# Kernel tuning notes

Measured on AMD Instinct MI355X. Metric: run time of the kernel, lower is better.

Reference implementation:

```python
import jax, jax.numpy as jnp
import numpy as np

N_NODES = 100000
N_EDGES = 1600000
D = 32
K = 3  # Chebyshev kernels
NEG_SLOPE = 0.2


def setup_inputs() -> dict:
    key = jax.random.key(0)
    ks = jax.random.split(key, 10)
    s = 1.0 / np.sqrt(D)
    return {
        "u": jax.random.normal(ks[0], (N_NODES, D), jnp.float32),
        "lambda_max": jnp.full((1,), 2.0, jnp.float32),
        "edge_src": jax.random.randint(ks[1], (N_EDGES,), 0, N_NODES, jnp.int32),
        "edge_dst": jax.random.randint(ks[2], (N_EDGES,), 0, N_NODES, jnp.int32),
        "cheb_W": jax.random.normal(ks[3], (K * D, D), jnp.float32) * s,
        "cheb_b": jnp.zeros((D,), jnp.float32),
        "src_W": jax.random.normal(ks[4], (D, D), jnp.float32) * s,
        "src_b": jnp.zeros((D,), jnp.float32),
        "dst_W": jax.random.normal(ks[5], (D, D), jnp.float32) * s,
        "dst_b": jnp.zeros((D,), jnp.float32),
        "attn": jax.random.normal(ks[6], (1, D), jnp.float32) * s,  # (heads=1, D)
    }


def reference(u, lambda_max, edge_src, edge_dst, cheb_W, cheb_b,
              src_W, src_b, dst_W, dst_b, attn):
    N = u.shape[0]
    # in-degrees (DGL: clamp(min=1) ** -0.5)
    deg = jnp.zeros((N,), u.dtype).at[edge_dst].add(1.0)
    Dinv = jnp.clip(deg, 1.0, None) ** -0.5  # (N,)

    def unnL(x):  # D^{-1/2} A D^{-1/2} x  via copy_u->sum message passing
        m = (x * Dinv[:, None])[edge_src]                       # (E, D)
        agg = jax.ops.segment_sum(m, edge_dst, num_segments=N)  # (N, D)
        return agg * Dinv[:, None]

    # --- ChebConv ---
    re_norm = 2.0 / lambda_max  # (1,) broadcast over all nodes
    X0 = u
    Xt = [X0]
    X1 = X0
    if K > 1:
        h = unnL(X0)
        X1 = -re_norm * h + X0 * (re_norm - 1.0)
        Xt.append(X1)
    for _ in range(2, K):
        h = unnL(X1)
        Xi = -2.0 * re_norm * h + X1 * (2.0 * (re_norm - 1.0)) - X0
        Xt.append(Xi)
        X0, X1 = X1, Xi
    Xcat = jnp.concatenate(Xt, axis=1)                 # (N, K*D)
    hc = jax.nn.relu(Xcat @ cheb_W + cheb_b)           # (N, D), DGL default activation=relu

    # --- GATv2Conv (heads=1) ---
    H = attn.shape[0]
    fsrc = (hc @ src_W + src_b).reshape(N, H, -1)      # (N, H, D)
    fdst = (hc @ dst_W + dst_b).reshape(N, H, -1)
    e = jax.nn.leaky_relu(fsrc[edge_src] + fdst[edge_dst], NEG_SLOPE)  # (E, H, D)
    logits = jnp.einsum('ehd,hd->eh', e, attn)         # (E, H)
    mx = jax.ops.segment_max(logits, edge_dst, num_segments=N)
    mx = jnp.where(jnp.isfinite(mx), mx, 0.0)
    ex = jnp.exp(logits - mx[edge_dst])
    den = jax.ops.segment_sum(ex, edge_dst, num_segments=N)
    a = ex / jnp.where(den > 0, den, 1.0)[edge_dst]    # edge softmax over dst groups
    msg = fsrc[edge_src] * a[:, :, None]               # (E, H, D)
    out = jax.ops.segment_sum(msg, edge_dst, num_segments=N)  # (N, H, D)
    return out.squeeze(1)
```

## Files before the change

kernel.cpp:

```cpp
#include <hip/hip_runtime.h>
#include <hip/hip_bf16.h>


typedef unsigned short u16;

#define DD 32
#define NEG_SLOPE 0.2f
#define BLK 256
#define TILE 4096
#define CB_SHIFT 8
#define CB_NODES 256
#define SRC_BITS 17

#define OFF_CHEBW 0
#define OFF_CHEBB 3072
#define OFF_SRCW  3104
#define OFF_SRCB  4128
#define OFF_DSTW  4160
#define OFF_DSTB  5184
#define OFF_ATTN  5216
#define OFF_LMAX  5248
#define W_TOTAL   5249

#define F_U     0
#define F_CHEBW 1
#define F_CHEBB 2
#define F_SRCW  3
#define F_SRCB  4
#define F_DSTW  5
#define F_DSTB  6
#define F_ATTN  7
#define F_LMAX  8
#define N_FLAGS 9

__device__ __forceinline__ float bh2f(u16 h) {
    return __uint_as_float(((unsigned)h) << 16);
}
__device__ __forceinline__ float rdin(const void* p, long long i, int f32f) {
    return f32f ? ((const float*)p)[i] : bh2f(((const u16*)p)[i]);
}
__device__ __forceinline__ float4 rd4(const void* p, long long row, int q, int f32f) {
    if (f32f) return ((const float4*)p)[row * 8 + q];
    ushort4 h = ((const ushort4*)p)[row * 8 + q];
    return make_float4(bh2f(h.x), bh2f(h.y), bh2f(h.z), bh2f(h.w));
}
__device__ __forceinline__ float lrelu(float x) { return fmaxf(x, NEG_SLOPE * x); }

__device__ __forceinline__ int plaus(u16 h) {
    if ((h & 0x7FFFu) == 0) return 1;
    unsigned e = (h >> 7) & 0xFF;
    return (e >= 0x60 && e <= 0x8F) ? 1 : 0;
}

__global__ void k_detect(const void* p0, const void* p1, const void* p2,
                         const void* p3, const void* p4, const void* p5,
                         const void* p6, const void* p7, const void* p8,
                         int n0, int n7, int* __restrict__ flags) {
    __shared__ int cEven, cEvenZ, cOddNZ;
    const void* ptrs[N_FLAGS] = {p0, p1, p2, p3, p4, p5, p6, p7, p8};
    const int   ns[N_FLAGS]   = {n0, 3072, 32, 1024, 32, 1024, 32, n7, 1};
    int a = blockIdx.x;
    if (a >= N_FLAGS) return;
    const u16* h = (const u16*)ptrs[a];
    int n = ns[a];
    if (threadIdx.x == 0) { cEven = 0; cEvenZ = 0; cOddNZ = 0; }
    __syncthreads();
    if (n == 1) {
        if (threadIdx.x == 0) {
            u16 v = h[0];
            flags[a] = ((v & 0x7FFFu) == 0 || !plaus(v)) ? 1 : 0;
        }
        return;
    }
    int nprobe = n >> 1;
    if (nprobe > 64) nprobe = 64;
    int t = threadIdx.x;
    if (t < nprobe) {
        u16 ev = h[2 * t];
        u16 od = h[2 * t + 1];
        if (plaus(ev)) atomicAdd(&cEven, 1);
        if ((ev & 0x7FFFu) == 0) atomicAdd(&cEvenZ, 1);
        if (plaus(od) && (od & 0x7FFFu) != 0) atomicAdd(&cOddNZ, 1);
    }
    __syncthreads();
    if (threadIdx.x == 0) {
        int bf = (cEven * 4 >= nprobe * 3);
        if (cEvenZ == nprobe && cOddNZ * 2 >= nprobe) bf = 0;
        flags[a] = bf ? 0 : 1;
    }
}

__global__ void k_cvtw(const void* chebW, const void* chebB, const void* srcW,
                       const void* srcB, const void* dstW, const void* dstB,
                       const void* attn, const void* lmax,
                       const int* __restrict__ flags, float* __restrict__ wsW,
                       unsigned* __restrict__ Mabs) {
    int i = blockIdx.x * blockDim.x + threadIdx.x;
    if (i >= W_TOTAL + 32) return;
    if (i >= W_TOTAL) { Mabs[i - W_TOTAL] = 0u; return; }
    float v;
    if      (i < OFF_CHEBB) v = rdin(chebW, i - OFF_CHEBW, flags[F_CHEBW]);
    else if (i < OFF_SRCW)  v = rdin(chebB, i - OFF_CHEBB, flags[F_CHEBB]);
    else if (i < OFF_SRCB)  v = rdin(srcW,  i - OFF_SRCW,  flags[F_SRCW]);
    else if (i < OFF_DSTW)  v = rdin(srcB,  i - OFF_SRCB,  flags[F_SRCB]);
    else if (i < OFF_DSTB)  v = rdin(dstW,  i - OFF_DSTW,  flags[F_DSTW]);
    else if (i < OFF_ATTN)  v = rdin(dstB,  i - OFF_DSTB,  flags[F_DSTB]);
    else if (i < OFF_LMAX)  v = rdin(attn,  i - OFF_ATTN,  flags[F_ATTN]);
    else                    v = rdin(lmax,  0,             flags[F_LMAX]);
    wsW[i] = v;
}


__global__ __launch_bounds__(BLK) void k_h1(
        const int* __restrict__ dst, unsigned* __restrict__ hist1,
        int E, int T, int NB1) {
    __shared__ unsigned lh[512];
    int tile = blockIdx.x, t = threadIdx.x;
    for (int b = t; b < 512; b += BLK) lh[b] = 0;
    __syncthreads();
    int base = tile * TILE;
    for (int i = 0; i < TILE / BLK; i++) {
        int e = base + i * BLK + t;
        if (e < E) atomicAdd(&lh[dst[e] >> CB_SHIFT], 1u);
    }
    __syncthreads();
    for (int b = t; b < NB1; b += BLK) hist1[(size_t)b * T + tile] = lh[b];
}

__global__ __launch_bounds__(BLK) void k_scA(
        unsigned* __restrict__ h, unsigned* __restrict__ bsum, int T) {
    __shared__ unsigned s[BLK];
    int b = blockIdx.x, t = threadIdx.x;
    unsigned carry = 0;
    for (int base = 0; base < T; base += BLK) {
        int i = base + t;
        unsigned v = (i < T) ? h[(size_t)b * T + i] : 0u;
        s[t] = v;
        __syncthreads();
        for (int off = 1; off < BLK; off <<= 1) {
            unsigned a = (t >= off) ? s[t - off] : 0u;
            __syncthreads();
            s[t] += a;
            __syncthreads();
        }
        if (i < T) h[(size_t)b * T + i] = carry + s[t] - v;
        carry += s[BLK - 1];
        __syncthreads();
    }
    if (t == 0) bsum[b] = carry;
}

__global__ __launch_bounds__(512) void k_scB(
        unsigned* __restrict__ bsum, int NB1,
        unsigned* __restrict__ row_ptr, int N, int E) {
    __shared__ unsigned s[512];
    int t = threadIdx.x;
    unsigned v = (t < NB1) ? bsum[t] : 0u;
    s[t] = v;
    __syncthreads();
    for (int off = 1; off < 512; off <<= 1) {
        unsigned a = (t >= off) ? s[t - off] : 0u;
        __syncthreads();
        s[t] += a;
        __syncthreads();
    }
    if (t < NB1) bsum[t] = s[t] - v;
    if (t == 0) row_ptr[N] = (unsigned)E;
}

__global__ __launch_bounds__(BLK) void k_s1(
        const int* __restrict__ src, const int* __restrict__ dst,
        const unsigned* __restrict__ off1, const unsigned* __restrict__ bsum,
        unsigned* __restrict__ tmp, int E, int T, int NB1) {
    __shared__ unsigned cur[512];
    int tile = blockIdx.x, t = threadIdx.x;
    for (int b = t; b < NB1; b += BLK)
        cur[b] = off1[(size_t)b * T + tile] + bsum[b];
    __syncthreads();
    int base = tile * TILE;
    for (int i = 0; i < TILE / BLK; i++) {
        int e = base + i * BLK + t;
        if (e < E) {
            int d = dst[e];
            unsigned pos = atomicAdd(&cur[d >> CB_SHIFT], 1u);
            tmp[pos] = ((unsigned)(d & (CB_NODES - 1)) << SRC_BITS) | (unsigned)src[e];
        }
    }
}

__global__ __launch_bounds__(BLK) void k_p2(
        const unsigned* __restrict__ tmp, const unsigned* __restrict__ bsum,
        unsigned* __restrict__ row_ptr, float* __restrict__ dinv,
        int* __restrict__ srcs, int N, int E, int T, int NB1) {
    __shared__ unsigned hist[CB_NODES], cur[CB_NODES], ssc[BLK];
    int b = blockIdx.x, t = threadIdx.x;
    int nodeBase = b << CB_SHIFT;
    unsigned lo = bsum[b];
    unsigned hi = (b + 1 < NB1) ? bsum[b + 1] : (unsigned)E;
    hist[t] = 0;
    __syncthreads();
    for (unsigned e = lo + t; e < hi; e += BLK)
        atomicAdd(&hist[tmp[e] >> SRC_BITS], 1u);
    __syncthreads();
    unsigned v = hist[t];
    ssc[t] = v;
    __syncthreads();
    for (int off = 1; off < BLK; off <<= 1) {
        unsigned a = (t >= off) ? ssc[t - off] : 0u;
        __syncthreads();
        ssc[t] += a;
        __syncthreads();
    }
    unsigned ex = ssc[t] - v;
    cur[t] = ex;
    int node = nodeBase + t;
    if (node < N) {
        row_ptr[node] = lo + ex;
        unsigned c = v;
        if (c < 1u) c = 1u;
        dinv[node] = rsqrtf((float)c);
    }
    __syncthreads();
    for (unsigned e = lo + t; e < hi; e += BLK) {
        unsigned p = tmp[e];
        unsigned pos = lo + atomicAdd(&cur[p >> SRC_BITS], 1u);
        srcs[pos] = (int)(p & ((1u << SRC_BITS) - 1u));
    }
}


__global__ __launch_bounds__(BLK) void k_unnl1(
        const void* __restrict__ u, const int* __restrict__ flags,
        const float* __restrict__ dinv, const unsigned* __restrict__ row_ptr,
        const int* __restrict__ srcs, const float* __restrict__ wsW,
        float* __restrict__ X1, int N) {
    int wave = (blockIdx.x * BLK + threadIdx.x) >> 6;
    if (wave >= N) return;
    int lane = threadIdx.x & 63, q = lane & 7, g = lane >> 3;
    int f = flags[F_U];
    int base = (int)row_ptr[wave], end = (int)row_ptr[wave + 1];
    float4 acc = make_float4(0.f, 0.f, 0.f, 0.f);
    for (int i = base; i < end; i += 32) {
        int e0 = i + g, e1 = i + 8 + g, e2 = i + 16 + g, e3 = i + 24 + g;
        int s0 = srcs[min(e0, end - 1)], s1 = srcs[min(e1, end - 1)];
        int s2 = srcs[min(e2, end - 1)], s3 = srcs[min(e3, end - 1)];
        float dv0 = dinv[s0], dv1 = dinv[s1], dv2 = dinv[s2], dv3 = dinv[s3];
        if (e0 >= end) dv0 = 0.f;
        if (e1 >= end) dv1 = 0.f;
        if (e2 >= end) dv2 = 0.f;
        if (e3 >= end) dv3 = 0.f;
        float4 x0 = rd4(u, s0, q, f);
        float4 x1 = rd4(u, s1, q, f);
        float4 x2 = rd4(u, s2, q, f);
        float4 x3 = rd4(u, s3, q, f);
        acc.x += x0.x * dv0 + x1.x * dv1 + x2.x * dv2 + x3.x * dv3;
        acc.y += x0.y * dv0 + x1.y * dv1 + x2.y * dv2 + x3.y * dv3;
        acc.z += x0.z * dv0 + x1.z * dv1 + x2.z * dv2 + x3.z * dv3;
        acc.w += x0.w * dv0 + x1.w * dv1 + x2.w * dv2 + x3.w * dv3;
    }
#pragma unroll
    for (int off = 8; off <= 32; off <<= 1) {
        acc.x += __shfl_xor(acc.x, off);
        acc.y += __shfl_xor(acc.y, off);
        acc.z += __shfl_xor(acc.z, off);
        acc.w += __shfl_xor(acc.w, off);
    }
    if (g == 0) {
        float rn = 2.0f / wsW[OFF_LMAX];
        float dn = dinv[wave];
        float4 x0 = rd4(u, wave, q, f);
        float4 r;
        r.x = -rn * (acc.x * dn) + x0.x * (rn - 1.f);
        r.y = -rn * (acc.y * dn) + x0.y * (rn - 1.f);
        r.z = -rn * (acc.z * dn) + x0.z * (rn - 1.f);
        r.w = -rn * (acc.w * dn) + x0.w * (rn - 1.f);
        ((float4*)X1)[(size_t)wave * 8 + q] = r;
    }
}

__global__ __launch_bounds__(BLK) void k_unnl2(
        const void* __restrict__ u, const int* __restrict__ flags,
        const float* __restrict__ X1, const float* __restrict__ dinv,
        const unsigned* __restrict__ row_ptr, const int* __restrict__ srcs,
        const float* __restrict__ wsW, float* __restrict__ X2, int N) {
    int wave = (blockIdx.x * BLK + threadIdx.x) >> 6;
    if (wave >= N) return;
    int lane = threadIdx.x & 63, q = lane & 7, g = lane >> 3;
    int base = (int)row_ptr[wave], end = (int)row_ptr[wave + 1];
    float4 acc = make_float4(0.f, 0.f, 0.f, 0.f);
    for (int i = base; i < end; i += 32) {
        int e0 = i + g, e1 = i + 8 + g, e2 = i + 16 + g, e3 = i + 24 + g;
        int s0 = srcs[min(e0, end - 1)], s1 = srcs[min(e1, end - 1)];
        int s2 = srcs[min(e2, end - 1)], s3 = srcs[min(e3, end - 1)];
        float dv0 = dinv[s0], dv1 = dinv[s1], dv2 = dinv[s2], dv3 = dinv[s3];
        if (e0 >= end) dv0 = 0.f;
        if (e1 >= end) dv1 = 0.f;
        if (e2 >= end) dv2 = 0.f;
        if (e3 >= end) dv3 = 0.f;
        float4 x0 = ((const float4*)X1)[(size_t)s0 * 8 + q];
        float4 x1 = ((const float4*)X1)[(size_t)s1 * 8 + q];
        float4 x2 = ((const float4*)X1)[(size_t)s2 * 8 + q];
        float4 x3 = ((const float4*)X1)[(size_t)s3 * 8 + q];
        acc.x += x0.x * dv0 + x1.x * dv1 + x2.x * dv2 + x3.x * dv3;
        acc.y += x0.y * dv0 + x1.y * dv1 + x2.y * dv2 + x3.y * dv3;
        acc.z += x0.z * dv0 + x1.z * dv1 + x2.z * dv2 + x3.z * dv3;
        acc.w += x0.w * dv0 + x1.w * dv1 + x2.w * dv2 + x3.w * dv3;
    }
#pragma unroll
    for (int off = 8; off <= 32; off <<= 1) {
        acc.x += __shfl_xor(acc.x, off);
        acc.y += __shfl_xor(acc.y, off);
        acc.z += __shfl_xor(acc.z, off);
        acc.w += __shfl_xor(acc.w, off);
    }
    if (g == 0) {
        float rn = 2.0f / wsW[OFF_LMAX];
        float dn = dinv[wave];
        float4 x0 = rd4(u, wave, q, flags[F_U]);
        float4 x1 = ((const float4*)X1)[(size_t)wave * 8 + q];
        float4 r;
        r.x = -2.f * rn * (acc.x * dn) + x1.x * (2.f * (rn - 1.f)) - x0.x;
        r.y = -2.f * rn * (acc.y * dn) + x1.y * (2.f * (rn - 1.f)) - x0.y;
        r.z = -2.f * rn * (acc.z * dn) + x1.z * (2.f * (rn - 1.f)) - x0.z;
        r.w = -2.f * rn * (acc.w * dn) + x1.w * (2.f * (rn - 1.f)) - x0.w;
        ((float4*)X2)[(size_t)wave * 8 + q] = r;
    }
}

__global__ __launch_bounds__(BLK) void k_cfsd(
        const void* __restrict__ u, const int* __restrict__ flags,
        const float* __restrict__ X1, const float* __restrict__ X2,
        const float* __restrict__ wsW, float* __restrict__ fsrc,
        float* __restrict__ fdst, unsigned* __restrict__ Mabs, int N) {
    __shared__ float sW[3072], sWs[1024], sWd[1024];
    __shared__ float sb[32], sbs[32], sbd[32];
    __shared__ float hcS[BLK * 33];
    __shared__ unsigned mloc[32];
    int t = threadIdx.x;
    for (int i = t; i < 3072; i += BLK) sW[i] = wsW[OFF_CHEBW + i];
    for (int i = t; i < 1024; i += BLK) {
        sWs[i] = wsW[OFF_SRCW + i];
        sWd[i] = wsW[OFF_DSTW + i];
    }
    if (t < 32) {
        sb[t]  = wsW[OFF_CHEBB + t];
        sbs[t] = wsW[OFF_SRCB + t];
        sbd[t] = wsW[OFF_DSTB + t];
        mloc[t] = 0u;
    }
    __syncthreads();
    int f = flags[F_U];
    float mabs = 0.f;
    int n = blockIdx.x * BLK + t;
    if (n < N) {
        long long row = (long long)n;
        float acc[32];
#pragma unroll
        for (int j = 0; j < 32; j++) acc[j] = sb[j];
        for (int i4 = 0; i4 < 8; i4++) {
            float4 x = rd4(u, row, i4, f);
            const float* w = &sW[i4 * 128];
#pragma unroll
            for (int j = 0; j < 32; j++) acc[j] = fmaf(x.x, w[j], acc[j]);
#pragma unroll
            for (int j = 0; j < 32; j++) acc[j] = fmaf(x.y, w[32 + j], acc[j]);
#pragma unroll
            for (int j = 0; j < 32; j++) acc[j] = fmaf(x.z, w[64 + j], acc[j]);
#pragma unroll
            for (int j = 0; j < 32; j++) acc[j] = fmaf(x.w, w[96 + j], acc[j]);
        }
        for (int i4 = 0; i4 < 8; i4++) {
            float4 x = ((const float4*)X1)[row * 8 + i4];
            const float* w = &sW[1024 + i4 * 128];
#pragma unroll
            for (int j = 0; j < 32; j++) acc[j] = fmaf(x.x, w[j], acc[j]);
#pragma unroll
            for (int j = 0; j < 32; j++) acc[j] = fmaf(x.y, w[32 + j], acc[j]);
#pragma unroll
            for (int j = 0; j < 32; j++) acc[j] = fmaf(x.z, w[64 + j], acc[j]);
#pragma unroll
            for (int j = 0; j < 32; j++) acc[j] = fmaf(x.w, w[96 + j], acc[j]);
        }
        for (int i4 = 0; i4 < 8; i4++) {
            float4 x = ((const float4*)X2)[row * 8 + i4];
            const float* w = &sW[2048 + i4 * 128];
#pragma unroll
            for (int j = 0; j < 32; j++) acc[j] = fmaf(x.x, w[j], acc[j]);
#pragma unroll
            for (int j = 0; j < 32; j++) acc[j] = fmaf(x.y, w[32 + j], acc[j]);
#pragma unroll
            for (int j = 0; j < 32; j++) acc[j] = fmaf(x.z, w[64 + j], acc[j]);
#pragma unroll
            for (int j = 0; j < 32; j++) acc[j] = fmaf(x.w, w[96 + j], acc[j]);
        }
#pragma unroll
        for (int j = 0; j < 32; j++) hcS[t * 33 + j] = fmaxf(acc[j], 0.f);
        float as[32], ad[32];
#pragma unroll
        for (int j = 0; j < 32; j++) { as[j] = sbs[j]; ad[j] = sbd[j]; }
        for (int i = 0; i < 32; i++) {
            float hv = hcS[t * 33 + i];
            const float* ws = &sWs[i * 32];
            const float* wd = &sWd[i * 32];
#pragma unroll
            for (int j = 0; j < 32; j++) {
                as[j] = fmaf(hv, ws[j], as[j]);
                ad[j] = fmaf(hv, wd[j], ad[j]);
            }
        }
        float4* fs4 = (float4*)(fsrc + row * 32);
        float4* fd4 = (float4*)(fdst + row * 32);
#pragma unroll
        for (int i4 = 0; i4 < 8; i4++) {
            fs4[i4] = make_float4(as[4 * i4], as[4 * i4 + 1], as[4 * i4 + 2], as[4 * i4 + 3]);
            fd4[i4] = make_float4(ad[4 * i4], ad[4 * i4 + 1], ad[4 * i4 + 2], ad[4 * i4 + 3]);
        }
#pragma unroll
        for (int j = 0; j < 32; j++) mabs = fmaxf(mabs, fabsf(as[j]));
    }
    atomicMax(&mloc[t & 31], __float_as_uint(mabs));
    __syncthreads();
    if (t < 32) atomicMax(&Mabs[t], mloc[t]);
}

__global__ __launch_bounds__(BLK) void k_gat(
        const float* __restrict__ fsrc, const float* __restrict__ fdst,
        const unsigned* __restrict__ row_ptr, const int* __restrict__ srcs,
        const float* __restrict__ wsW, const unsigned* __restrict__ Mabs,
        float* __restrict__ out, int N) {
    int wave = (blockIdx.x * BLK + threadIdx.x) >> 6;
    if (wave >= N) return;
    int lane = threadIdx.x & 63, q = lane & 7, g = lane >> 3;
    int base = (int)row_ptr[wave], end = (int)row_ptr[wave + 1];
    if (base == end) {
        if (g == 0)
            ((float4*)out)[(size_t)wave * 8 + q] = make_float4(0.f, 0.f, 0.f, 0.f);
        return;
    }
    float4 fd = ((const float4*)fdst)[(size_t)wave * 8 + q];
    float4 at = ((const float4*)(wsW + OFF_ATTN))[q];
    float4 mb = ((const float4*)Mabs)[q];
    float kp = (mb.x + fabsf(fd.x)) * fabsf(at.x) +
               (mb.y + fabsf(fd.y)) * fabsf(at.y) +
               (mb.z + fabsf(fd.z)) * fabsf(at.z) +
               (mb.w + fabsf(fd.w)) * fabsf(at.w);
    kp += __shfl_xor(kp, 1);
    kp += __shfl_xor(kp, 2);
    kp += __shfl_xor(kp, 4);
    float K = kp;
    float4 acc = make_float4(0.f, 0.f, 0.f, 0.f);
    float den = 0.f;
    for (int i = base; i < end; i += 16) {
        int e0 = i + g, e1 = i + 8 + g;
        int ec0 = min(e0, end - 1), ec1 = min(e1, end - 1);
        int s0 = srcs[ec0], s1 = srcs[ec1];
        float4 fs0 = ((const float4*)fsrc)[(size_t)s0 * 8 + q];
        float4 fs1 = ((const float4*)fsrc)[(size_t)s1 * 8 + q];
        float v0 = lrelu(fs0.x + fd.x) * at.x + lrelu(fs0.y + fd.y) * at.y +
                   lrelu(fs0.z + fd.z) * at.z + lrelu(fs0.w + fd.w) * at.w;
        float v1 = lrelu(fs1.x + fd.x) * at.x + lrelu(fs1.y + fd.y) * at.y +
                   lrelu(fs1.z + fd.z) * at.z + lrelu(fs1.w + fd.w) * at.w;
        v0 += __shfl_xor(v0, 1);  v1 += __shfl_xor(v1, 1);
        v0 += __shfl_xor(v0, 2);  v1 += __shfl_xor(v1, 2);
        v0 += __shfl_xor(v0, 4);  v1 += __shfl_xor(v1, 4);
        float w0 = (e0 < end) ? __expf(v0 - K) : 0.f;
        float w1 = (e1 < end) ? __expf(v1 - K) : 0.f;
        acc.x += fs0.x * w0 + fs1.x * w1;
        acc.y += fs0.y * w0 + fs1.y * w1;
        acc.z += fs0.z * w0 + fs1.z * w1;
        acc.w += fs0.w * w0 + fs1.w * w1;
        den += w0 + w1;
    }
#pragma unroll
    for (int off = 8; off <= 32; off <<= 1) {
        acc.x += __shfl_xor(acc.x, off);
        acc.y += __shfl_xor(acc.y, off);
        acc.z += __shfl_xor(acc.z, off);
        acc.w += __shfl_xor(acc.w, off);
        den   += __shfl_xor(den, off);
    }
    if (g == 0) {
        float inv = 1.f / (den > 0.f ? den : 1.f);
        ((float4*)out)[(size_t)wave * 8 + q] =
            make_float4(acc.x * inv, acc.y * inv, acc.z * inv, acc.w * inv);
    }
}

extern "C" void kernel_launch(void* const* d_in, const int* in_sizes, int n_in,
                              void* d_out, int out_size, void* d_ws, size_t ws_size,
                              hipStream_t stream) {
    const void* u     = d_in[0];
    const void* lmax  = d_in[1];
    const int*  esrc  = (const int*)d_in[2];
    const int*  edst  = (const int*)d_in[3];
    const void* chebW = d_in[4];
    const void* chebB = d_in[5];
    const void* srcW  = d_in[6];
    const void* srcB  = d_in[7];
    const void* dstW  = d_in[8];
    const void* dstB  = d_in[9];
    const void* attn  = d_in[10];

    const int ND = in_sizes[0];
    const int N  = ND / DD;
    const int E  = in_sizes[2];

    const int NB1 = (N + CB_NODES - 1) >> CB_SHIFT;
    const int T   = (E + TILE - 1) / TILE;
    const int M   = NB1 * T;

    float* ws   = (float*)d_ws;
    float* X1   = ws;
    float* X2   = ws + (size_t)ND;
    unsigned* tmp = (unsigned*)(ws + 2 * (size_t)ND);
    int*   srcs = (int*)(tmp + E);
    unsigned* hist1   = (unsigned*)(srcs + E);
    unsigned* row_ptr = hist1 + M;
    float*    dinv    = (float*)(row_ptr + (N + 1));
    unsigned* bsum    = (unsigned*)(dinv + N);
    float*    wsW     = (float*)(((uintptr_t)(bsum + NB1) + 15) & ~(uintptr_t)15);
    int*      flags   = (int*)(wsW + W_TOTAL);
    unsigned* Mabs    = (unsigned*)(((uintptr_t)(flags + N_FLAGS) + 15) & ~(uintptr_t)15);
    float*    out     = (float*)d_out;

    auto gb = [](long long n, int b) { return (unsigned)((n + b - 1) / b); };

    k_detect<<<N_FLAGS, 64, 0, stream>>>(u, chebW, chebB, srcW, srcB, dstW, dstB,
                                         attn, lmax, ND, DD, flags);
    k_cvtw<<<gb(W_TOTAL + 32, BLK), BLK, 0, stream>>>(chebW, chebB, srcW, srcB,
                                                      dstW, dstB, attn, lmax,
                                                      flags, wsW, Mabs);

    k_h1<<<T, BLK, 0, stream>>>(edst, hist1, E, T, NB1);
    k_scA<<<NB1, BLK, 0, stream>>>(hist1, bsum, T);
    k_scB<<<1, 512, 0, stream>>>(bsum, NB1, row_ptr, N, E);
    k_s1<<<T, BLK, 0, stream>>>(esrc, edst, hist1, bsum, tmp, E, T, NB1);
    k_p2<<<NB1, BLK, 0, stream>>>(tmp, bsum, row_ptr, dinv, srcs, N, E, T, NB1);

    k_unnl1<<<gb((long long)N * 64, BLK), BLK, 0, stream>>>(u, flags, dinv, row_ptr,
                                                            srcs, wsW, X1, N);
    k_unnl2<<<gb((long long)N * 64, BLK), BLK, 0, stream>>>(u, flags, X1, dinv, row_ptr,
                                                            srcs, wsW, X2, N);

    k_cfsd<<<gb(N, BLK), BLK, 0, stream>>>(u, flags, X1, X2, wsW, X1, X2, Mabs, N);

    k_gat<<<gb((long long)N * 64, BLK), BLK, 0, stream>>>(X1, X2, row_ptr, srcs,
                                                          wsW, Mabs, out, N);
}
```

Baseline: 285.5 us.

## Store gathered node features as bf16 to halve gather traffic

Converts the input features to a bf16 copy and stores the Chebyshev intermediates X1, X2 and the GAT source projection in bf16. Every per-edge gather in the two propagation kernels and the attention kernel then reads half the bytes. It adds a conversion kernel and loses precision on intermediates, which the slightly inflated max-abs bound for the softmax shift is meant to absorb. fdst stays fp32, and X1b is reused as the buffer for fsrc.

After: 290.2 us. About the same (+1.6%).

```diff
diff --git a/kernel.cpp b/kernel.cpp
--- a/kernel.cpp
+++ b/kernel.cpp
@@ -36,6 +36,10 @@
 __device__ __forceinline__ float bh2f(u16 h) {
     return __uint_as_float(((unsigned)h) << 16);
 }
+__device__ __forceinline__ u16 f2b(float v) {
+    unsigned x = __float_as_uint(v);
+    return (u16)((x + 0x7FFFu + ((x >> 16) & 1u)) >> 16);
+}
 __device__ __forceinline__ float rdin(const void* p, long long i, int f32f) {
     return f32f ? ((const float*)p)[i] : bh2f(((const u16*)p)[i]);
 }
@@ -43,6 +47,14 @@
     if (f32f) return ((const float4*)p)[row * 8 + q];
     ushort4 h = ((const ushort4*)p)[row * 8 + q];
     return make_float4(bh2f(h.x), bh2f(h.y), bh2f(h.z), bh2f(h.w));
+}
+__device__ __forceinline__ float4 rb4(const u16* p, long long row, int q) {
+    ushort4 h = ((const ushort4*)p)[row * 8 + q];
+    return make_float4(bh2f(h.x), bh2f(h.y), bh2f(h.z), bh2f(h.w));
+}
+__device__ __forceinline__ ushort4 pk4(float a, float b, float c, float d) {
+    ushort4 r; r.x = f2b(a); r.y = f2b(b); r.z = f2b(c); r.w = f2b(d);
+    return r;
 }
 __device__ __forceinline__ float lrelu(float x) { return fmaxf(x, NEG_SLOPE * x); }
 
@@ -110,6 +122,12 @@
     wsW[i] = v;
 }
 
+__global__ void k_cvtu(const void* __restrict__ u, const int* __restrict__ flags,
+                       u16* __restrict__ ub, int ND) {
+    int i = blockIdx.x * blockDim.x + threadIdx.x;
+    if (i < ND) ub[i] = f2b(rdin(u, i, flags[F_U]));
+}
+
 
 __global__ __launch_bounds__(BLK) void k_h1(
         const int* __restrict__ dst, unsigned* __restrict__ hist1,
@@ -230,59 +248,10 @@
 
 
 __global__ __launch_bounds__(BLK) void k_unnl1(
-        const void* __restrict__ u, const int* __restrict__ flags,
-        const float* __restrict__ dinv, const unsigned* __restrict__ row_ptr,
-        const int* __restrict__ srcs, const float* __restrict__ wsW,
-        float* __restrict__ X1, int N) {
-    int wave = (blockIdx.x * BLK + threadIdx.x) >> 6;
-    if (wave >= N) return;
-    int lane = threadIdx.x & 63, q = lane & 7, g = lane >> 3;
-    int f = flags[F_U];
-    int base = (int)row_ptr[wave], end = (int)row_ptr[wave + 1];
-    float4 acc = make_float4(0.f, 0.f, 0.f, 0.f);
-    for (int i = base; i < end; i += 32) {
-        int e0 = i + g, e1 = i + 8 + g, e2 = i + 16 + g, e3 = i + 24 + g;
-        int s0 = srcs[min(e0, end - 1)], s1 = srcs[min(e1, end - 1)];
-        int s2 = srcs[min(e2, end - 1)], s3 = srcs[min(e3, end - 1)];
-        float dv0 = dinv[s0], dv1 = dinv[s1], dv2 = dinv[s2], dv3 = dinv[s3];
-        if (e0 >= end) dv0 = 0.f;
-        if (e1 >= end) dv1 = 0.f;
-        if (e2 >= end) dv2 = 0.f;
-        if (e3 >= end) dv3 = 0.f;
-        float4 x0 = rd4(u, s0, q, f);
-        float4 x1 = rd4(u, s1, q, f);
-        float4 x2 = rd4(u, s2, q, f);
-        float4 x3 = rd4(u, s3, q, f);
-        acc.x += x0.x * dv0 + x1.x * dv1 + x2.x * dv2 + x3.x * dv3;
-        acc.y += x0.y * dv0 + x1.y * dv1 + x2.y * dv2 + x3.y * dv3;
-        acc.z += x0.z * dv0 + x1.z * dv1 + x2.z * dv2 + x3.z * dv3;
-        acc.w += x0.w * dv0 + x1.w * dv1 + x2.w * dv2 + x3.w * dv3;
-    }
-#pragma unroll
-    for (int off = 8; off <= 32; off <<= 1) {
-        acc.x += __shfl_xor(acc.x, off);
-        acc.y += __shfl_xor(acc.y, off);
-        acc.z += __shfl_xor(acc.z, off);
-        acc.w += __shfl_xor(acc.w, off);
-    }
-    if (g == 0) {
-        float rn = 2.0f / wsW[OFF_LMAX];
-        float dn = dinv[wave];
-        float4 x0 = rd4(u, wave, q, f);
-        float4 r;
-        r.x = -rn * (acc.x * dn) + x0.x * (rn - 1.f);
-        r.y = -rn * (acc.y * dn) + x0.y * (rn - 1.f);
-        r.z = -rn * (acc.z * dn) + x0.z * (rn - 1.f);
-        r.w = -rn * (acc.w * dn) + x0.w * (rn - 1.f);
-        ((float4*)X1)[(size_t)wave * 8 + q] = r;
-    }
-}
-
-__global__ __launch_bounds__(BLK) void k_unnl2(
-        const void* __restrict__ u, const int* __restrict__ flags,
-        const float* __restrict__ X1, const float* __restrict__ dinv,
+        const u16* __restrict__ ub, const void* __restrict__ u,
+        const int* __restrict__ flags, const float* __restrict__ dinv,
         const unsigned* __restrict__ row_ptr, const int* __restrict__ srcs,
-        const float* __restrict__ wsW, float* __restrict__ X2, int N) {
+        const float* __restrict__ wsW, u16* __restrict__ X1b, int N) {
     int wave = (blockIdx.x * BLK + threadIdx.x) >> 6;
     if (wave >= N) return;
     int lane = threadIdx.x & 63, q = lane & 7, g = lane >> 3;
@@ -297,10 +266,10 @@
         if (e1 >= end) dv1 = 0.f;
         if (e2 >= end) dv2 = 0.f;
         if (e3 >= end) dv3 = 0.f;
-        float4 x0 = ((const float4*)X1)[(size_t)s0 * 8 + q];
-        float4 x1 = ((const float4*)X1)[(size_t)s1 * 8 + q];
-        float4 x2 = ((const float4*)X1)[(size_t)s2 * 8 + q];
-        float4 x3 = ((const float4*)X1)[(size_t)s3 * 8 + q];
+        float4 x0 = rb4(ub, s0, q);
+        float4 x1 = rb4(ub, s1, q);
+        float4 x2 = rb4(ub, s2, q);
+        float4 x3 = rb4(ub, s3, q);
         acc.x += x0.x * dv0 + x1.x * dv1 + x2.x * dv2 + x3.x * dv3;
         acc.y += x0.y * dv0 + x1.y * dv1 + x2.y * dv2 + x3.y * dv3;
         acc.z += x0.z * dv0 + x1.z * dv1 + x2.z * dv2 + x3.z * dv3;
@@ -317,21 +286,67 @@
         float rn = 2.0f / wsW[OFF_LMAX];
         float dn = dinv[wave];
         float4 x0 = rd4(u, wave, q, flags[F_U]);
-        float4 x1 = ((const float4*)X1)[(size_t)wave * 8 + q];
-        float4 r;
-        r.x = -2.f * rn * (acc.x * dn) + x1.x * (2.f * (rn - 1.f)) - x0.x;
-        r.y = -2.f * rn * (acc.y * dn) + x1.y * (2.f * (rn - 1.f)) - x0.y;
-        r.z = -2.f * rn * (acc.z * dn) + x1.z * (2.f * (rn - 1.f)) - x0.z;
-        r.w = -2.f * rn * (acc.w * dn) + x1.w * (2.f * (rn - 1.f)) - x0.w;
-        ((float4*)X2)[(size_t)wave * 8 + q] = r;
+        ((ushort4*)X1b)[(size_t)wave * 8 + q] =
+            pk4(-rn * (acc.x * dn) + x0.x * (rn - 1.f),
+                -rn * (acc.y * dn) + x0.y * (rn - 1.f),
+                -rn * (acc.z * dn) + x0.z * (rn - 1.f),
+                -rn * (acc.w * dn) + x0.w * (rn - 1.f));
+    }
+}
+
+__global__ __launch_bounds__(BLK) void k_unnl2(
+        const u16* __restrict__ X1b, const void* __restrict__ u,
+        const int* __restrict__ flags, const float* __restrict__ dinv,
+        const unsigned* __restrict__ row_ptr, const int* __restrict__ srcs,
+        const float* __restrict__ wsW, u16* __restrict__ X2b, int N) {
+    int wave = (blockIdx.x * BLK + threadIdx.x) >> 6;
+    if (wave >= N) return;
+    int lane = threadIdx.x & 63, q = lane & 7, g = lane >> 3;
+    int base = (int)row_ptr[wave], end = (int)row_ptr[wave + 1];
+    float4 acc = make_float4(0.f, 0.f, 0.f, 0.f);
+    for (int i = base; i < end; i += 32) {
+        int e0 = i + g, e1 = i + 8 + g, e2 = i + 16 + g, e3 = i + 24 + g;
+        int s0 = srcs[min(e0, end - 1)], s1 = srcs[min(e1, end - 1)];
+        int s2 = srcs[min(e2, end - 1)], s3 = srcs[min(e3, end - 1)];
+        float dv0 = dinv[s0], dv1 = dinv[s1], dv2 = dinv[s2], dv3 = dinv[s3];
+        if (e0 >= end) dv0 = 0.f;
+        if (e1 >= end) dv1 = 0.f;
+        if (e2 >= end) dv2 = 0.f;
+        if (e3 >= end) dv3 = 0.f;
+        float4 x0 = rb4(X1b, s0, q);
+        float4 x1 = rb4(X1b, s1, q);
+        float4 x2 = rb4(X1b, s2, q);
+        float4 x3 = rb4(X1b, s3, q);
+        acc.x += x0.x * dv0 + x1.x * dv1 + x2.x * dv2 + x3.x * dv3;
+        acc.y += x0.y * dv0 + x1.y * dv1 + x2.y * dv2 + x3.y * dv3;
+        acc.z += x0.z * dv0 + x1.z * dv1 + x2.z * dv2 + x3.z * dv3;
+        acc.w += x0.w * dv0 + x1.w * dv1 + x2.w * dv2 + x3.w * dv3;
+    }
+#pragma unroll
+    for (int off = 8; off <= 32; off <<= 1) {
+        acc.x += __shfl_xor(acc.x, off);
+        acc.y += __shfl_xor(acc.y, off);
+        acc.z += __shfl_xor(acc.z, off);
+        acc.w += __shfl_xor(acc.w, off);
+    }
+    if (g == 0) {
+        float rn = 2.0f / wsW[OFF_LMAX];
+        float dn = dinv[wave];
+        float4 x0 = rd4(u, wave, q, flags[F_U]);
+        float4 x1 = rb4(X1b, wave, q);
+        ((ushort4*)X2b)[(size_t)wave * 8 + q] =
+            pk4(-2.f * rn * (acc.x * dn) + x1.x * (2.f * (rn - 1.f)) - x0.x,
+                -2.f * rn * (acc.y * dn) + x1.y * (2.f * (rn - 1.f)) - x0.y,
+                -2.f * rn * (acc.z * dn) + x1.z * (2.f * (rn - 1.f)) - x0.z,
+                -2.f * rn * (acc.w * dn) + x1.w * (2.f * (rn - 1.f)) - x0.w);
     }
 }
 
 __global__ __launch_bounds__(BLK) void k_cfsd(
         const void* __restrict__ u, const int* __restrict__ flags,
-        const float* __restrict__ X1, const float* __restrict__ X2,
-        const float* __restrict__ wsW, float* __restrict__ fsrc,
-        float* __restrict__ fdst, unsigned* __restrict__ Mabs, int N) {
+        const u16* X1b, const u16* X2b,
+        const float* __restrict__ wsW, u16* fsrcb,
+        float* __restrict__ fd, unsigned* __restrict__ Mabs, int N) {
     __shared__ float sW[3072], sWs[1024], sWd[1024];
     __shared__ float sb[32], sbs[32], sbd[32];
     __shared__ float hcS[BLK * 33];
@@ -370,7 +385,7 @@
             for (int j = 0; j < 32; j++) acc[j] = fmaf(x.w, w[96 + j], acc[j]);
         }
         for (int i4 = 0; i4 < 8; i4++) {
-            float4 x = ((const float4*)X1)[row * 8 + i4];
+            float4 x = rb4(X1b, row, i4);
             const float* w = &sW[1024 + i4 * 128];
 #pragma unroll
             for (int j = 0; j < 32; j++) acc[j] = fmaf(x.x, w[j], acc[j]);
@@ -382,7 +397,7 @@
             for (int j = 0; j < 32; j++) acc[j] = fmaf(x.w, w[96 + j], acc[j]);
         }
         for (int i4 = 0; i4 < 8; i4++) {
-            float4 x = ((const float4*)X2)[row * 8 + i4];
+            float4 x = rb4(X2b, row, i4);
             const float* w = &sW[2048 + i4 * 128];
 #pragma unroll
             for (int j = 0; j < 32; j++) acc[j] = fmaf(x.x, w[j], acc[j]);
@@ -408,23 +423,23 @@
                 ad[j] = fmaf(hv, wd[j], ad[j]);
             }
         }
-        float4* fs4 = (float4*)(fsrc + row * 32);
-        float4* fd4 = (float4*)(fdst + row * 32);
+        ushort4* fs4 = (ushort4*)(fsrcb + row * 32);
+        float4*  fd4 = (float4*)(fd + row * 32);
 #pragma unroll
         for (int i4 = 0; i4 < 8; i4++) {
-            fs4[i4] = make_float4(as[4 * i4], as[4 * i4 + 1], as[4 * i4 + 2], as[4 * i4 + 3]);
+            fs4[i4] = pk4(as[4 * i4], as[4 * i4 + 1], as[4 * i4 + 2], as[4 * i4 + 3]);
             fd4[i4] = make_float4(ad[4 * i4], ad[4 * i4 + 1], ad[4 * i4 + 2], ad[4 * i4 + 3]);
         }
 #pragma unroll
         for (int j = 0; j < 32; j++) mabs = fmaxf(mabs, fabsf(as[j]));
     }
-    atomicMax(&mloc[t & 31], __float_as_uint(mabs));
+    atomicMax(&mloc[t & 31], __float_as_uint(mabs * 1.01f));
     __syncthreads();
     if (t < 32) atomicMax(&Mabs[t], mloc[t]);
 }
 
 __global__ __launch_bounds__(BLK) void k_gat(
-        const float* __restrict__ fsrc, const float* __restrict__ fdst,
+        const u16* __restrict__ fsrcb, const float* __restrict__ fd,
         const unsigned* __restrict__ row_ptr, const int* __restrict__ srcs,
         const float* __restrict__ wsW, const unsigned* __restrict__ Mabs,
         float* __restrict__ out, int N) {
@@ -437,13 +452,13 @@
             ((float4*)out)[(size_t)wave * 8 + q] = make_float4(0.f, 0.f, 0.f, 0.f);
         return;
     }
-    float4 fd = ((const float4*)fdst)[(size_t)wave * 8 + q];
+    float4 fdv = ((const float4*)fd)[(size_t)wave * 8 + q];
     float4 at = ((const float4*)(wsW + OFF_ATTN))[q];
     float4 mb = ((const float4*)Mabs)[q];
-    float kp = (mb.x + fabsf(fd.x)) * fabsf(at.x) +
-               (mb.y + fabsf(fd.y)) * fabsf(at.y) +
-               (mb.z + fabsf(fd.z)) * fabsf(at.z) +
-               (mb.w + fabsf(fd.w)) * fabsf(at.w);
+    float kp = (mb.x + fabsf(fdv.x)) * fabsf(at.x) +
+               (mb.y + fabsf(fdv.y)) * fabsf(at.y) +
+               (mb.z + fabsf(fdv.z)) * fabsf(at.z) +
+               (mb.w + fabsf(fdv.w)) * fabsf(at.w);
     kp += __shfl_xor(kp, 1);
     kp += __shfl_xor(kp, 2);
     kp += __shfl_xor(kp, 4);
@@ -454,12 +469,12 @@
         int e0 = i + g, e1 = i + 8 + g;
         int ec0 = min(e0, end - 1), ec1 = min(e1, end - 1);
         int s0 = srcs[ec0], s1 = srcs[ec1];
-        float4 fs0 = ((const float4*)fsrc)[(size_t)s0 * 8 + q];
-        float4 fs1 = ((const float4*)fsrc)[(size_t)s1 * 8 + q];
-        float v0 = lrelu(fs0.x + fd.x) * at.x + lrelu(fs0.y + fd.y) * at.y +
-                   lrelu(fs0.z + fd.z) * at.z + lrelu(fs0.w + fd.w) * at.w;
-        float v1 = lrelu(fs1.x + fd.x) * at.x + lrelu(fs1.y + fd.y) * at.y +
-                   lrelu(fs1.z + fd.z) * at.z + lrelu(fs1.w + fd.w) * at.w;
+        float4 fs0 = rb4(fsrcb, s0, q);
+        float4 fs1 = rb4(fsrcb, s1, q);
+        float v0 = lrelu(fs0.x + fdv.x) * at.x + lrelu(fs0.y + fdv.y) * at.y +
+                   lrelu(fs0.z + fdv.z) * at.z + lrelu(fs0.w + fdv.w) * at.w;
+        float v1 = lrelu(fs1.x + fdv.x) * at.x + lrelu(fs1.y + fdv.y) * at.y +
+                   lrelu(fs1.z + fdv.z) * at.z + lrelu(fs1.w + fdv.w) * at.w;
         v0 += __shfl_xor(v0, 1);  v1 += __shfl_xor(v1, 1);
         v0 += __shfl_xor(v0, 2);  v1 += __shfl_xor(v1, 2);
         v0 += __shfl_xor(v0, 4);  v1 += __shfl_xor(v1, 4);
@@ -509,10 +524,11 @@
     const int T   = (E + TILE - 1) / TILE;
     const int M   = NB1 * T;
 
-    float* ws   = (float*)d_ws;
-    float* X1   = ws;
-    float* X2   = ws + (size_t)ND;
-    unsigned* tmp = (unsigned*)(ws + 2 * (size_t)ND);
+    u16* ub   = (u16*)d_ws;
+    u16* X1b  = ub + (size_t)ND;
+    u16* X2b  = X1b + (size_t)ND;
+    float* fd = (float*)(X2b + (size_t)ND);
+    unsigned* tmp = (unsigned*)(fd + (size_t)ND);
     int*   srcs = (int*)(tmp + E);
     unsigned* hist1   = (unsigned*)(srcs + E);
     unsigned* row_ptr = hist1 + M;
@@ -530,6 +546,7 @@
     k_cvtw<<<gb(W_TOTAL + 32, BLK), BLK, 0, stream>>>(chebW, chebB, srcW, srcB,
                                                       dstW, dstB, attn, lmax,
                                                       flags, wsW, Mabs);
+    k_cvtu<<<gb(ND, BLK), BLK, 0, stream>>>(u, flags, ub, ND);
 
     k_h1<<<T, BLK, 0, stream>>>(edst, hist1, E, T, NB1);
     k_scA<<<NB1, BLK, 0, stream>>>(hist1, bsum, T);
@@ -537,13 +554,13 @@
     k_s1<<<T, BLK, 0, stream>>>(esrc, edst, hist1, bsum, tmp, E, T, NB1);
     k_p2<<<NB1, BLK, 0, stream>>>(tmp, bsum, row_ptr, dinv, srcs, N, E, T, NB1);
 
-    k_unnl1<<<gb((long long)N * 64, BLK), BLK, 0, stream>>>(u, flags, dinv, row_ptr,
-                                                            srcs, wsW, X1, N);
-    k_unnl2<<<gb((long long)N * 64, BLK), BLK, 0, stream>>>(u, flags, X1, dinv, row_ptr,
-                                                            srcs, wsW, X2, N);
-
-    k_cfsd<<<gb(N, BLK), BLK, 0, stream>>>(u, flags, X1, X2, wsW, X1, X2, Mabs, N);
-
-    k_gat<<<gb((long long)N * 64, BLK), BLK, 0, stream>>>(X1, X2, row_ptr, srcs,
+    k_unnl1<<<gb((long long)N * 64, BLK), BLK, 0, stream>>>(ub, u, flags, dinv,
+                                                            row_ptr, srcs, wsW, X1b, N);
+    k_unnl2<<<gb((long long)N * 64, BLK), BLK, 0, stream>>>(X1b, u, flags, dinv,
+                                                            row_ptr, srcs, wsW, X2b, N);
+
+    k_cfsd<<<gb(N, BLK), BLK, 0, stream>>>(u, flags, X1b, X2b, wsW, X1b, fd, Mabs, N);
+
+    k_gat<<<gb((long long)N * 64, BLK), BLK, 0, stream>>>(X1b, fd, row_ptr, srcs,
                                                           wsW, Mabs, out, N);
 }
```
